# Kernel tuning notes

Hardware: AMD Instinct MI355X
Metric: run time of the kernel (lower is better)

## Reference

```python
import jax, jax.numpy as jnp
import numpy as np

SIGMA = 0.05  # gaussian bandwidth from the source


def _sqdist(a, b):
    # a: [B,N,D], b: [B,M,D] -> [B,N,M] squared euclidean distance
    a2 = jnp.sum(a * a, axis=-1)[:, :, None]
    b2 = jnp.sum(b * b, axis=-1)[:, None, :]
    return a2 + b2 - 2.0 * jnp.einsum('bnd,bmd->bnm', a, b)


def setup_inputs() -> dict:
    key = jax.random.key(0)
    k1, k2, k3, k4 = jax.random.split(key, 4)
    B, N, D = 2, 4096, 32
    points = jax.random.normal(k1, (B, N, 3), dtype=jnp.float32)
    pointfea1 = jax.random.normal(k2, (B, N, D), dtype=jnp.float32)
    pointfea2 = jax.random.normal(k3, (B, N, D), dtype=jnp.float32)
    weights = jax.random.uniform(k4, (B, N), dtype=jnp.float32) / N  # point-cloud mass weights
    return {"points": points, "pointfea1": pointfea1, "pointfea2": pointfea2, "weights": weights}


def reference(points, pointfea1, pointfea2, weights):
    # naive_corres: per-point spatial log-gaussian softmax vs feature log-softmax,
    # weighted squared difference, reduced over both pair axes -> [B]
    x = points / SIGMA
    point_loggauss = jax.nn.log_softmax(-_sqdist(x, x), axis=2)          # [B,N,N]
    fea_logsoftmax = jax.nn.log_softmax(-_sqdist(pointfea1, pointfea2), axis=2)  # [B,N,N]
    diff2 = (jnp.exp(point_loggauss) - jnp.exp(fea_logsoftmax)) ** 2
    l2_loss = jnp.sum(diff2 * weights[:, :, None], axis=2)  # sum over j
    return jnp.sum(l2_loss, axis=1)                          # sum over i -> [B]
```

## Files before the change

### kernel.cpp

```cpp
#include <hip/hip_runtime.h>

#define D    32
#define BLK  256
#define NCH  16
#define SJ   128

#define LOG2E 1.44269504088896340736f

typedef short  short8  __attribute__((ext_vector_type(8)));
typedef float  floatx4 __attribute__((ext_vector_type(4)));
typedef float  v2f     __attribute__((ext_vector_type(2)));

__device__ __forceinline__ short f2bf(float v) {
    union { float f; unsigned u; } x; x.f = v;
    unsigned r = x.u + 0x7fffu + ((x.u >> 16) & 1u);
    return (short)(r >> 16);
}
__device__ __forceinline__ float bf2f(short h) {
    union { float f; unsigned u; } x;
    x.u = ((unsigned)(unsigned short)h) << 16;
    return x.f;
}
__device__ __forceinline__ float fast_exp2(float x) {
#if __has_builtin(__builtin_amdgcn_exp2f)
    return __builtin_amdgcn_exp2f(x);
#else
    return exp2f(x);
#endif
}

__global__ __launch_bounds__(BLK) void precompute_kernel(
    const float* __restrict__ points,
    const float* __restrict__ fea1,
    const float* __restrict__ fea2,
    float4* __restrict__ xp,
    float* __restrict__ f1n,
    float* __restrict__ f2n,
    short* __restrict__ f2hi,
    short* __restrict__ f2lo,
    float* __restrict__ acc,
    float* __restrict__ out,
    int BN, int Bsz)
{
    int r = blockIdx.x * BLK + threadIdx.x;
    if (r < Bsz) out[r] = 0.0f;
    if (r >= BN) return;
#pragma unroll
    for (int s = 0; s < 5; ++s) acc[s * BN + r] = 0.0f;

    const float s20 = 20.0f;
    float x = points[3*r+0] * s20;
    float y = points[3*r+1] * s20;
    float z = points[3*r+2] * s20;
    float4 v; v.x = x; v.y = y; v.z = z;
    v.w = (x*x + y*y + z*z) * LOG2E;
    xp[r] = v;

    const float4* p1 = (const float4*)(fea1 + (size_t)r * D);
    float n1 = 0.f;
#pragma unroll
    for (int k = 0; k < D/4; ++k) {
        float4 a = p1[k];
        n1 = fmaf(a.x,a.x, fmaf(a.y,a.y, fmaf(a.z,a.z, fmaf(a.w,a.w, n1))));
    }
    f1n[r] = n1 * LOG2E;

    const int t = r >> 4;
    const int m = r & 15;
    const float* p2 = fea2 + (size_t)r * D;
    float n2 = 0.f;
#pragma unroll
    for (int q = 0; q < 4; ++q) {
        float4 v0 = *(const float4*)(p2 + q*8);
        float4 v1 = *(const float4*)(p2 + q*8 + 4);
        float e[8] = {v0.x,v0.y,v0.z,v0.w,v1.x,v1.y,v1.z,v1.w};
        short8 h, l;
#pragma unroll
        for (int k = 0; k < 8; ++k) {
            n2 = fmaf(e[k], e[k], n2);
            short hh = f2bf(e[k]);
            h[k] = hh;
            l[k] = f2bf(e[k] - bf2f(hh));
        }
        size_t off = ((size_t)t * 64 + m + 16*q) * 8;
        *(short8*)&f2hi[off] = h;
        *(short8*)&f2lo[off] = l;
    }
    f2n[r] = n2 * LOG2E;
}

__global__ __launch_bounds__(BLK) void pair_kernel(
    const float* __restrict__ fea1,
    const short* __restrict__ f2hi,
    const short* __restrict__ f2lo,
    const float4* __restrict__ xp,
    const float* __restrict__ f1n,
    const float* __restrict__ f2n,
    float* __restrict__ acc,
    int N, int BN)
{
    __shared__ __align__(16) short sHi[SJ * D];
    __shared__ __align__(16) short sLo[SJ * D];
    __shared__ float4 sXJ[SJ];
    __shared__ float  sFN[SJ];

    const int tid  = threadIdx.x;
    const int lane = tid & 63;
    const int wv   = tid >> 6;
    const int m    = lane & 15;
    const int q    = lane >> 4;

    const int ibpb  = N / 64;
    const int b     = blockIdx.x / ibpb;
    const int ibase = blockIdx.x * 64 + wv * 16;
    const int JCH   = N / NCH;
    const int jc0   = blockIdx.y * JCH;

    const float* f1p = fea1 + (size_t)(ibase + m) * D + q * 8;
    float4 bv0 = *(const float4*)(f1p);
    float4 bv1 = *(const float4*)(f1p + 4);
    float bfv[8] = {bv0.x,bv0.y,bv0.z,bv0.w,bv1.x,bv1.y,bv1.z,bv1.w};
    short8 F1hi, F1lo;
#pragma unroll
    for (int k = 0; k < 8; ++k) {
        short h = f2bf(bfv[k]);
        F1hi[k] = h;
        F1lo[k] = f2bf(bfv[k] - bf2f(h));
    }

    const float L2 = 2.0f * LOG2E;
    v2f vxx[2], vxy[2], vxz[2], vmw[2], vnf[2];
#pragma unroll
    for (int g = 0; g < 2; ++g) {
        int i0 = ibase + q*4 + g*2;
        float4 a0 = xp[i0];
        float4 a1 = xp[i0 + 1];
        v2f t;
        t.x = a0.x * L2; t.y = a1.x * L2; vxx[g] = t;
        t.x = a0.y * L2; t.y = a1.y * L2; vxy[g] = t;
        t.x = a0.z * L2; t.y = a1.z * L2; vxz[g] = t;
        t.x = -a0.w;     t.y = -a1.w;     vmw[g] = t;
        t.x = -f1n[i0];  t.y = -f1n[i0+1]; vnf[g] = t;
    }
    v2f vL2 = {L2, L2};

    v2f sA2[2]  = {{0.f,0.f},{0.f,0.f}};
    v2f sB2[2]  = {{0.f,0.f},{0.f,0.f}};
    v2f s2a2[2] = {{0.f,0.f},{0.f,0.f}};
    v2f s2b2[2] = {{0.f,0.f},{0.f,0.f}};
    v2f sab2[2] = {{0.f,0.f},{0.f,0.f}};

    const short*  gHi  = f2hi + ((size_t)(b * N + jc0) >> 4) * 512;
    const short*  gLo  = f2lo + ((size_t)(b * N + jc0) >> 4) * 512;
    const float4* xpb  = xp  + (size_t)b * N + jc0;
    const float*  f2nb = f2n + (size_t)b * N + jc0;

    for (int s = 0; s < JCH; s += SJ) {
        const uint4* srcH = (const uint4*)(gHi + (size_t)(s >> 4) * 512);
        const uint4* srcL = (const uint4*)(gLo + (size_t)(s >> 4) * 512);
        uint4* dstH = (uint4*)sHi;
        uint4* dstL = (uint4*)sLo;
        dstH[tid]       = srcH[tid];
        dstH[tid + 256] = srcH[tid + 256];
        dstL[tid]       = srcL[tid];
        dstL[tid + 256] = srcL[tid + 256];
        if (tid < SJ) {
            sXJ[tid] = xpb[s + tid];
            sFN[tid] = f2nb[s + tid];
        }
        __syncthreads();

#pragma unroll 2
        for (int jt8 = 0; jt8 < SJ/16; ++jt8) {
            const short8 Ahi = *(const short8*)&sHi[(jt8 * 64 + lane) * 8];
            const short8 Alo = *(const short8*)&sLo[(jt8 * 64 + lane) * 8];
            floatx4 c = {0.f, 0.f, 0.f, 0.f};
            c = __builtin_amdgcn_mfma_f32_16x16x32_bf16(F1hi, Ahi, c, 0, 0, 0);
            c = __builtin_amdgcn_mfma_f32_16x16x32_bf16(F1hi, Alo, c, 0, 0, 0);
            c = __builtin_amdgcn_mfma_f32_16x16x32_bf16(F1lo, Ahi, c, 0, 0, 0);

            const int jl = jt8 * 16 + m;
            float4 xj = sXJ[jl];
            float fnj = sFN[jl];
            v2f xx = {xj.x, xj.x};
            v2f yy = {xj.y, xj.y};
            v2f zz = {xj.z, xj.z};
            v2f ww = {xj.w, xj.w};
            v2f ff = {fnj, fnj};

#pragma unroll
            for (int g = 0; g < 2; ++g) {
                v2f c2; c2.x = c[g*2]; c2.y = c[g*2 + 1];
                v2f t0 = __builtin_elementwise_fma(xx, vxx[g], vmw[g]);
                t0 = __builtin_elementwise_fma(yy, vxy[g], t0);
                t0 = __builtin_elementwise_fma(zz, vxz[g], t0);
                v2f aL = t0 - ww;
                v2f bL = __builtin_elementwise_fma(c2, vL2, vnf[g] - ff);
                v2f ea; ea.x = fast_exp2(aL.x); ea.y = fast_exp2(aL.y);
                v2f eb; eb.x = fast_exp2(bL.x); eb.y = fast_exp2(bL.y);
                sA2[g]  += ea;
                sB2[g]  += eb;
                s2a2[g] = __builtin_elementwise_fma(ea, ea, s2a2[g]);
                s2b2[g] = __builtin_elementwise_fma(eb, eb, s2b2[g]);
                sab2[g] = __builtin_elementwise_fma(ea, eb, sab2[g]);
            }
        }
        __syncthreads();
    }

#define RED2(v) do {                                                       \
        v.x += __shfl_xor(v.x, 1); v.x += __shfl_xor(v.x, 2);              \
        v.x += __shfl_xor(v.x, 4); v.x += __shfl_xor(v.x, 8);              \
        v.y += __shfl_xor(v.y, 1); v.y += __shfl_xor(v.y, 2);              \
        v.y += __shfl_xor(v.y, 4); v.y += __shfl_xor(v.y, 8);              \
    } while (0)
#pragma unroll
    for (int g = 0; g < 2; ++g) {
        RED2(sA2[g]); RED2(s2a2[g]); RED2(sB2[g]); RED2(s2b2[g]); RED2(sab2[g]);
    }
#undef RED2

    if (m < 4) {
        int row = ibase + q*4 + m;
#define PICK(arr) ((m & 1) ? ((m & 2) ? arr[1].y : arr[0].y)               \
                           : ((m & 2) ? arr[1].x : arr[0].x))
        atomicAdd(&acc[0*BN + row], PICK(sA2));
        atomicAdd(&acc[1*BN + row], PICK(s2a2));
        atomicAdd(&acc[2*BN + row], PICK(sB2));
        atomicAdd(&acc[3*BN + row], PICK(s2b2));
        atomicAdd(&acc[4*BN + row], PICK(sab2));
#undef PICK
    }
}

__global__ __launch_bounds__(BLK) void finalize_kernel(
    const float* __restrict__ acc,
    const float* __restrict__ weights,
    float* __restrict__ out,
    int N, int BN)
{
    int row = blockIdx.x * BLK + threadIdx.x;
    int b   = (blockIdx.x * BLK) / N;

    float A   = acc[0*BN + row];
    float S2a = acc[1*BN + row];
    float Bt  = acc[2*BN + row];
    float S2b = acc[3*BN + row];
    float Sab = acc[4*BN + row];
    float invA = 1.0f / A;
    float invB = 1.0f / Bt;
    float val  = S2a*invA*invA - 2.0f*Sab*invA*invB + S2b*invB*invB;
    float sum  = weights[row] * val;

    __shared__ float red[BLK/64];
    for (int off = 32; off > 0; off >>= 1)
        sum += __shfl_down(sum, off);
    if ((threadIdx.x & 63) == 0) red[threadIdx.x >> 6] = sum;
    __syncthreads();
    if (threadIdx.x == 0) {
        float s = 0.f;
#pragma unroll
        for (int w = 0; w < BLK/64; ++w) s += red[w];
        atomicAdd(&out[b], s);
    }
}

extern "C" void kernel_launch(void* const* d_in, const int* in_sizes, int n_in,
                              void* d_out, int out_size, void* d_ws, size_t ws_size,
                              hipStream_t stream) {
    const float* points  = (const float*)d_in[0];
    const float* fea1    = (const float*)d_in[1];
    const float* fea2    = (const float*)d_in[2];
    const float* weights = (const float*)d_in[3];
    float* out = (float*)d_out;

    int B  = out_size;
    int BN = in_sizes[3];
    int N  = BN / B;

    float*  acc  = (float*)d_ws;
    float4* xp   = (float4*)((char*)d_ws + (size_t)5  * BN * 4);
    float*  f2n  = (float*)((char*)d_ws + (size_t)9  * BN * 4);
    float*  f1n  = (float*)((char*)d_ws + (size_t)10 * BN * 4);
    short*  f2hi = (short*)((char*)d_ws + (size_t)11 * BN * 4);
    short*  f2lo = f2hi + (size_t)BN * D;

    precompute_kernel<<<dim3((BN + BLK - 1) / BLK), dim3(BLK), 0, stream>>>(
        points, fea1, fea2, xp, f1n, f2n, f2hi, f2lo, acc, out, BN, B);

    dim3 grid(BN / 64, NCH);
    pair_kernel<<<grid, dim3(BLK), 0, stream>>>(
        fea1, f2hi, f2lo, xp, f1n, f2n, acc, N, BN);

    finalize_kernel<<<dim3(BN / BLK), dim3(BLK), 0, stream>>>(acc, weights, out, N, BN);
}
```

Baseline: 88.86 us.

## Reduce pair partials through shared memory and cut per-row atomics

The pair kernel's final reduction changes. It does one xor-8 shuffle step, writes the partial sums to shared memory (reusing the tile buffers), then lets 80 threads sum 8 partials and issue vectorised-row atomics. This replaces the full 4-step shuffle tree and per-lane atomics. The precompute kernel now stores the negated norms so the inner loop does an add instead of a subtract, runs with 64-thread blocks for more parallel blocks, and the pair kernel gains a launch_bounds occupancy hint of 8. The cost is an extra block barrier at the end, and the occupancy hint may cap register use.

```diff
diff --git a/kernel.cpp b/kernel.cpp
--- a/kernel.cpp
+++ b/kernel.cpp
@@ -2,6 +2,7 @@
 
 #define D    32
 #define BLK  256
+#define BLKP 64
 #define NCH  16
 #define SJ   128
 
@@ -29,20 +30,20 @@
 #endif
 }
 
-__global__ __launch_bounds__(BLK) void precompute_kernel(
+__global__ __launch_bounds__(BLKP) void precompute_kernel(
     const float* __restrict__ points,
     const float* __restrict__ fea1,
     const float* __restrict__ fea2,
-    float4* __restrict__ xp,
+    float4* __restrict__ xp4,
     float* __restrict__ f1n,
-    float* __restrict__ f2n,
+    float* __restrict__ mfn,
     short* __restrict__ f2hi,
     short* __restrict__ f2lo,
     float* __restrict__ acc,
     float* __restrict__ out,
     int BN, int Bsz)
 {
-    int r = blockIdx.x * BLK + threadIdx.x;
+    int r = blockIdx.x * BLKP + threadIdx.x;
     if (r < Bsz) out[r] = 0.0f;
     if (r >= BN) return;
 #pragma unroll
@@ -53,8 +54,8 @@
     float y = points[3*r+1] * s20;
     float z = points[3*r+2] * s20;
     float4 v; v.x = x; v.y = y; v.z = z;
-    v.w = (x*x + y*y + z*z) * LOG2E;
-    xp[r] = v;
+    v.w = -((x*x + y*y + z*z) * LOG2E);
+    xp4[r] = v;
 
     const float4* p1 = (const float4*)(fea1 + (size_t)r * D);
     float n1 = 0.f;
@@ -86,23 +87,25 @@
         *(short8*)&f2hi[off] = h;
         *(short8*)&f2lo[off] = l;
     }
-    f2n[r] = n2 * LOG2E;
-}
-
-__global__ __launch_bounds__(BLK) void pair_kernel(
+    mfn[r] = -(n2 * LOG2E);
+}
+
+__global__ __launch_bounds__(BLK, 8) void pair_kernel(
     const float* __restrict__ fea1,
     const short* __restrict__ f2hi,
     const short* __restrict__ f2lo,
-    const float4* __restrict__ xp,
+    const float4* __restrict__ xp4,
     const float* __restrict__ f1n,
-    const float* __restrict__ f2n,
+    const float* __restrict__ mfn,
     float* __restrict__ acc,
     int N, int BN)
 {
-    __shared__ __align__(16) short sHi[SJ * D];
-    __shared__ __align__(16) short sLo[SJ * D];
-    __shared__ float4 sXJ[SJ];
-    __shared__ float  sFN[SJ];
+    __shared__ __align__(16) char smem[8192 + 8192 + 2048 + 512];
+    short*  sHi = (short*)smem;
+    short*  sLo = (short*)(smem + 8192);
+    float4* sXJ = (float4*)(smem + 16384);
+    float*  sFN = (float*)(smem + 18432);
+    float*  sRED = (float*)smem;
 
     const int tid  = threadIdx.x;
     const int lane = tid & 63;
@@ -133,13 +136,13 @@
 #pragma unroll
     for (int g = 0; g < 2; ++g) {
         int i0 = ibase + q*4 + g*2;
-        float4 a0 = xp[i0];
-        float4 a1 = xp[i0 + 1];
+        float4 a0 = xp4[i0];
+        float4 a1 = xp4[i0 + 1];
         v2f t;
         t.x = a0.x * L2; t.y = a1.x * L2; vxx[g] = t;
         t.x = a0.y * L2; t.y = a1.y * L2; vxy[g] = t;
         t.x = a0.z * L2; t.y = a1.z * L2; vxz[g] = t;
-        t.x = -a0.w;     t.y = -a1.w;     vmw[g] = t;
+        t.x = a0.w;      t.y = a1.w;      vmw[g] = t;
         t.x = -f1n[i0];  t.y = -f1n[i0+1]; vnf[g] = t;
     }
     v2f vL2 = {L2, L2};
@@ -150,10 +153,10 @@
     v2f s2b2[2] = {{0.f,0.f},{0.f,0.f}};
     v2f sab2[2] = {{0.f,0.f},{0.f,0.f}};
 
-    const short*  gHi  = f2hi + ((size_t)(b * N + jc0) >> 4) * 512;
-    const short*  gLo  = f2lo + ((size_t)(b * N + jc0) >> 4) * 512;
-    const float4* xpb  = xp  + (size_t)b * N + jc0;
-    const float*  f2nb = f2n + (size_t)b * N + jc0;
+    const short*  gHi = f2hi + ((size_t)(b * N + jc0) >> 4) * 512;
+    const short*  gLo = f2lo + ((size_t)(b * N + jc0) >> 4) * 512;
+    const float4* xpb = xp4 + (size_t)b * N + jc0;
+    const float*  fnb = mfn + (size_t)b * N + jc0;
 
     for (int s = 0; s < JCH; s += SJ) {
         const uint4* srcH = (const uint4*)(gHi + (size_t)(s >> 4) * 512);
@@ -166,7 +169,7 @@
         dstL[tid + 256] = srcL[tid + 256];
         if (tid < SJ) {
             sXJ[tid] = xpb[s + tid];
-            sFN[tid] = f2nb[s + tid];
+            sFN[tid] = fnb[s + tid];
         }
         __syncthreads();
 
@@ -182,24 +185,24 @@
             const int jl = jt8 * 16 + m;
             float4 xj = sXJ[jl];
             float fnj = sFN[jl];
-            v2f xx = {xj.x, xj.x};
-            v2f yy = {xj.y, xj.y};
-            v2f zz = {xj.z, xj.z};
-            v2f ww = {xj.w, xj.w};
-            v2f ff = {fnj, fnj};
+            v2f xjx = {xj.x, xj.x};
+            v2f xjy = {xj.y, xj.y};
+            v2f xjz = {xj.z, xj.z};
+            v2f xjw = {xj.w, xj.w};
+            v2f fn2 = {fnj, fnj};
 
 #pragma unroll
             for (int g = 0; g < 2; ++g) {
-                v2f c2; c2.x = c[g*2]; c2.y = c[g*2 + 1];
-                v2f t0 = __builtin_elementwise_fma(xx, vxx[g], vmw[g]);
-                t0 = __builtin_elementwise_fma(yy, vxy[g], t0);
-                t0 = __builtin_elementwise_fma(zz, vxz[g], t0);
-                v2f aL = t0 - ww;
-                v2f bL = __builtin_elementwise_fma(c2, vL2, vnf[g] - ff);
+                v2f c2; c2.x = c[2*g]; c2.y = c[2*g + 1];
+                v2f t0 = __builtin_elementwise_fma(xjx, vxx[g], vmw[g]);
+                t0 = __builtin_elementwise_fma(xjy, vxy[g], t0);
+                t0 = __builtin_elementwise_fma(xjz, vxz[g], t0);
+                v2f aL = t0 + xjw;
+                v2f bL = __builtin_elementwise_fma(c2, vL2, vnf[g] + fn2);
                 v2f ea; ea.x = fast_exp2(aL.x); ea.y = fast_exp2(aL.y);
                 v2f eb; eb.x = fast_exp2(bL.x); eb.y = fast_exp2(bL.y);
-                sA2[g]  += ea;
-                sB2[g]  += eb;
+                sA2[g] += ea;
+                sB2[g] += eb;
                 s2a2[g] = __builtin_elementwise_fma(ea, ea, s2a2[g]);
                 s2b2[g] = __builtin_elementwise_fma(eb, eb, s2b2[g]);
                 sab2[g] = __builtin_elementwise_fma(ea, eb, sab2[g]);
@@ -208,28 +211,41 @@
         __syncthreads();
     }
 
-#define RED2(v) do {                                                       \
-        v.x += __shfl_xor(v.x, 1); v.x += __shfl_xor(v.x, 2);              \
-        v.x += __shfl_xor(v.x, 4); v.x += __shfl_xor(v.x, 8);              \
-        v.y += __shfl_xor(v.y, 1); v.y += __shfl_xor(v.y, 2);              \
-        v.y += __shfl_xor(v.y, 4); v.y += __shfl_xor(v.y, 8);              \
-    } while (0)
-#pragma unroll
-    for (int g = 0; g < 2; ++g) {
-        RED2(sA2[g]); RED2(s2a2[g]); RED2(sB2[g]); RED2(s2b2[g]); RED2(sab2[g]);
-    }
-#undef RED2
-
-    if (m < 4) {
-        int row = ibase + q*4 + m;
-#define PICK(arr) ((m & 1) ? ((m & 2) ? arr[1].y : arr[0].y)               \
-                           : ((m & 2) ? arr[1].x : arr[0].x))
-        atomicAdd(&acc[0*BN + row], PICK(sA2));
-        atomicAdd(&acc[1*BN + row], PICK(s2a2));
-        atomicAdd(&acc[2*BN + row], PICK(sB2));
-        atomicAdd(&acc[3*BN + row], PICK(s2b2));
-        atomicAdd(&acc[4*BN + row], PICK(sab2));
-#undef PICK
+#define F8(v) do { v.x += __shfl_xor(v.x, 8); v.y += __shfl_xor(v.y, 8); } while (0)
+    F8(sA2[0]);  F8(sA2[1]);
+    F8(s2a2[0]); F8(s2a2[1]);
+    F8(sB2[0]);  F8(sB2[1]);
+    F8(s2b2[0]); F8(s2b2[1]);
+    F8(sab2[0]); F8(sab2[1]);
+#undef F8
+
+    if (m < 8) {
+        float* base = sRED + (size_t)((wv*4 + q) * 5) * 40 + m * 4;
+        float4 t;
+        t.x=sA2[0].x;  t.y=sA2[0].y;  t.z=sA2[1].x;  t.w=sA2[1].y;  *(float4*)(base + 0*40) = t;
+        t.x=s2a2[0].x; t.y=s2a2[0].y; t.z=s2a2[1].x; t.w=s2a2[1].y; *(float4*)(base + 1*40) = t;
+        t.x=sB2[0].x;  t.y=sB2[0].y;  t.z=sB2[1].x;  t.w=sB2[1].y;  *(float4*)(base + 2*40) = t;
+        t.x=s2b2[0].x; t.y=s2b2[0].y; t.z=s2b2[1].x; t.w=s2b2[1].y; *(float4*)(base + 3*40) = t;
+        t.x=sab2[0].x; t.y=sab2[0].y; t.z=sab2[1].x; t.w=sab2[1].y; *(float4*)(base + 4*40) = t;
+    }
+    __syncthreads();
+
+    if (tid < 80) {
+        const float* rbase = sRED + (size_t)tid * 40;
+        float4 sm = *(const float4*)(rbase);
+#pragma unroll
+        for (int mm = 1; mm < 8; ++mm) {
+            float4 t = *(const float4*)(rbase + mm * 4);
+            sm.x += t.x; sm.y += t.y; sm.z += t.z; sm.w += t.w;
+        }
+        int iq  = tid / 5;
+        int qty = tid - iq * 5;
+        int row = blockIdx.x * 64 + iq * 4;
+        float* ap = acc + (size_t)qty * BN + row;
+        atomicAdd(ap + 0, sm.x);
+        atomicAdd(ap + 1, sm.y);
+        atomicAdd(ap + 2, sm.z);
+        atomicAdd(ap + 3, sm.w);
     }
 }
 
@@ -279,18 +295,18 @@
     int N  = BN / B;
 
     float*  acc  = (float*)d_ws;
-    float4* xp   = (float4*)((char*)d_ws + (size_t)5  * BN * 4);
-    float*  f2n  = (float*)((char*)d_ws + (size_t)9  * BN * 4);
+    float4* xp4  = (float4*)((char*)d_ws + (size_t)5  * BN * 4);
+    float*  mfn  = (float*)((char*)d_ws + (size_t)9  * BN * 4);
     float*  f1n  = (float*)((char*)d_ws + (size_t)10 * BN * 4);
     short*  f2hi = (short*)((char*)d_ws + (size_t)11 * BN * 4);
     short*  f2lo = f2hi + (size_t)BN * D;
 
-    precompute_kernel<<<dim3((BN + BLK - 1) / BLK), dim3(BLK), 0, stream>>>(
-        points, fea1, fea2, xp, f1n, f2n, f2hi, f2lo, acc, out, BN, B);
+    precompute_kernel<<<dim3((BN + BLKP - 1) / BLKP), dim3(BLKP), 0, stream>>>(
+        points, fea1, fea2, xp4, f1n, mfn, f2hi, f2lo, acc, out, BN, B);
 
     dim3 grid(BN / 64, NCH);
     pair_kernel<<<grid, dim3(BLK), 0, stream>>>(
-        fea1, f2hi, f2lo, xp, f1n, f2n, acc, N, BN);
+        fea1, f2hi, f2lo, xp4, f1n, mfn, acc, N, BN);
 
     finalize_kernel<<<dim3(BN / BLK), dim3(BLK), 0, stream>>>(acc, weights, out, N, BN);
 }
```

New measurement: 183.4 us. 106% more time.
